# Performance work log

Measured on AMD Instinct MI355X. Metric: run time of the kernel, lower is better.

## Reference

```python
import jax, jax.numpy as jnp
import numpy as np

T, B, I, H, O = 256, 128, 512, 1024, 1


def setup_inputs() -> dict:
    key = jax.random.key(0)
    ks = jax.random.split(key, 7)
    s_ih = 1.0 / np.sqrt(H)
    return {
        "x": jax.random.normal(ks[0], (T, B, I), dtype=jnp.float32),
        "W_ih": jax.random.normal(ks[1], (H, I), dtype=jnp.float32) * s_ih,
        "W_hh": jax.random.normal(ks[2], (H, H), dtype=jnp.float32) * s_ih,
        "b_ih": jax.random.normal(ks[3], (H,), dtype=jnp.float32) * s_ih,
        "b_hh": jax.random.normal(ks[4], (H,), dtype=jnp.float32) * s_ih,
        "W_fc": jax.random.normal(ks[5], (O, H), dtype=jnp.float32) * s_ih,
        "b_fc": jax.random.normal(ks[6], (O,), dtype=jnp.float32) * s_ih,
    }


def reference(x, W_ih, W_hh, b_ih, b_hh, W_fc, b_fc):
    # Precompute the input projection for all timesteps at once: [T, B, H]
    xp = jnp.einsum("tbi,hi->tbh", x, W_ih) + b_ih + b_hh
    W_hh_T = W_hh.T  # [H, H]

    def step(h, xp_t):
        # h: [B, H]; torch nn.RNN uses tanh nonlinearity by default
        h_new = jnp.tanh(xp_t + h @ W_hh_T)
        return h_new, h_new

    h0 = jnp.zeros((B, H), dtype=x.dtype)  # hidden0 = zeros in the module
    _, hs = jax.lax.scan(step, h0, xp)  # hs: [T, B, H]

    # Linear head over every timestep's hidden state: [T, B, O]
    return jnp.einsum("tbh,oh->tbo", hs, W_fc) + b_fc
```

## Files before the change

kernel.cpp:

```cpp
#include <hip/hip_runtime.h>
#include <stdint.h>

typedef __attribute__((ext_vector_type(8))) short short8;
typedef __attribute__((ext_vector_type(4))) float f32x4;
typedef __attribute__((ext_vector_type(4))) unsigned int u32x4;
typedef __attribute__((ext_vector_type(2))) unsigned int u32x2;

__device__ __forceinline__ unsigned short f2bf(float f) {
  unsigned u = __float_as_uint(f);
  u += 0x7FFFu + ((u >> 16) & 1u);
  return (unsigned short)(u >> 16);
}
__device__ __forceinline__ float bf2f(unsigned short s) {
  return __uint_as_float(((unsigned)s) << 16);
}
__device__ __forceinline__ float ftanh(float x) {
  float e = __expf(2.0f * x);
  return 1.0f - 2.0f / (e + 1.0f);
}

__global__ __launch_bounds__(256) void cvt_kernel(const float* __restrict__ in,
                                                  unsigned short* __restrict__ out,
                                                  int n8) {
  int i = blockIdx.x * 256 + threadIdx.x;
  if (i >= n8) return;
  const float4* p = (const float4*)in + (size_t)i * 2;
  float4 a = p[0], b = p[1];
  uint4 o;
  o.x = (unsigned)f2bf(a.x) | ((unsigned)f2bf(a.y) << 16);
  o.y = (unsigned)f2bf(a.z) | ((unsigned)f2bf(a.w) << 16);
  o.z = (unsigned)f2bf(b.x) | ((unsigned)f2bf(b.y) << 16);
  o.w = (unsigned)f2bf(b.z) | ((unsigned)f2bf(b.w) << 16);
  ((uint4*)out)[i] = o;
}

__global__ __launch_bounds__(256) void scrub_kernel(unsigned* __restrict__ dst,
                                                    int n4) {
  int i = blockIdx.x * 256 + threadIdx.x;
  if (i >= n4) return;
  ((u32x4*)dst)[i] = (u32x4){0xAAAAAAAAu, 0xAAAAAAAAu, 0xAAAAAAAAu, 0xAAAAAAAAu};
}

__global__ __launch_bounds__(256) void gemm_xp(const unsigned short* __restrict__ A,
                                               const unsigned short* __restrict__ Bw,
                                               const float* __restrict__ b_ih,
                                               const float* __restrict__ b_hh,
                                               unsigned short* __restrict__ xp) {
  __shared__ unsigned short Al[8192];
  __shared__ unsigned short Bl[8192];
  int tid = threadIdx.x, lane = tid & 63, w = tid >> 6;
  int wm = w & 1, wn = w >> 1;
  int bx = blockIdx.x;
  int m0 = (bx >> 3) * 128, n0 = (bx & 7) * 128;

  f32x4 acc[4][4];
#pragma unroll
  for (int i = 0; i < 4; ++i)
#pragma unroll
    for (int jq = 0; jq < 4; ++jq) acc[i][jq] = (f32x4){0.f, 0.f, 0.f, 0.f};

  for (int kb = 0; kb < 512; kb += 64) {
#pragma unroll
    for (int i = 0; i < 4; ++i) {
      int S = (w * 4 + i) * 64 + lane;
      int row = S >> 3, pg = S & 7;
      int gk = ((pg ^ (row & 7)) << 3);
      const unsigned short* ga = A + (size_t)(m0 + row) * 512 + kb + gk;
      const unsigned short* gb = Bw + (size_t)(n0 + row) * 512 + kb + gk;
      __builtin_amdgcn_global_load_lds(
          (const __attribute__((address_space(1))) unsigned int*)ga,
          (__attribute__((address_space(3))) unsigned int*)&Al[(size_t)((w * 4 + i) * 64) * 8],
          16, 0, 0);
      __builtin_amdgcn_global_load_lds(
          (const __attribute__((address_space(1))) unsigned int*)gb,
          (__attribute__((address_space(3))) unsigned int*)&Bl[(size_t)((w * 4 + i) * 64) * 8],
          16, 0, 0);
    }
    asm volatile("s_waitcnt vmcnt(0)" ::: "memory");
    __syncthreads();

#pragma unroll
    for (int c = 0; c < 2; ++c) {
      short8 av[4], bv[4];
      int gg = c * 4 + (lane >> 4);
#pragma unroll
      for (int mt = 0; mt < 4; ++mt) {
        int rowa = wm * 64 + mt * 16 + (lane & 15);
        av[mt] = *(const short8*)&Al[(rowa * 8 + (gg ^ (rowa & 7))) * 8];
        int rowb = wn * 64 + mt * 16 + (lane & 15);
        bv[mt] = *(const short8*)&Bl[(rowb * 8 + (gg ^ (rowb & 7))) * 8];
      }
#pragma unroll
      for (int mt = 0; mt < 4; ++mt)
#pragma unroll
        for (int nt = 0; nt < 4; ++nt)
          acc[mt][nt] = __builtin_amdgcn_mfma_f32_16x16x32_bf16(av[mt], bv[nt], acc[mt][nt], 0, 0, 0);
    }
    __syncthreads();
  }

  int cl = lane & 15, qd = lane >> 4;
#pragma unroll
  for (int nt = 0; nt < 4; ++nt) {
    int col = n0 + wn * 64 + nt * 16 + cl;
    float bias = b_ih[col] + b_hh[col];
#pragma unroll
    for (int mt = 0; mt < 4; ++mt) {
#pragma unroll
      for (int r = 0; r < 4; ++r) {
        int m = m0 + wm * 64 + mt * 16 + qd * 4 + r;
        xp[(size_t)m * 1024 + col] = f2bf(acc[mt][nt][r] + bias);
      }
    }
  }
}

__global__ __launch_bounds__(512, 1) void scan_kernel(
    const float* __restrict__ Whh, const unsigned short* __restrict__ xp,
    const float* __restrict__ Wfc, const float* __restrict__ bfc,
    unsigned short* __restrict__ hs, float* __restrict__ out) {
  __shared__ __align__(16) unsigned short Abuf[2][2048 * 8];
  const int tid = threadIdx.x;
  const int lane = tid & 63, w = tid >> 6;
  const int g = blockIdx.x >> 3, p = blockIdx.x & 7;
  const int r = lane & 15, q = lane >> 4;
  const int b0 = g * 16;
  const int tile = p * 128 + w * 16;
  const int gcol = tile + r;
  const float bfcv = bfc[0];
  const float4 wfc4 = *(const float4*)(Wfc + tile + q * 4);
  const unsigned short* xlane = xp + (size_t)(b0 + r) * 1024 + tile + q * 4;

  int o0, o1, o2, o3;
  {
    int m, l, c, bb, q2;
    m = tid;         l = m & 63; c = m >> 6; bb = l & 15; q2 = l >> 4;
    o0 = (b0 + bb) * 1024 + c * 32 + q2 * 8;
    m = tid + 512;   l = m & 63; c = m >> 6; bb = l & 15; q2 = l >> 4;
    o1 = (b0 + bb) * 1024 + c * 32 + q2 * 8;
    m = tid + 1024;  l = m & 63; c = m >> 6; bb = l & 15; q2 = l >> 4;
    o2 = (b0 + bb) * 1024 + c * 32 + q2 * 8;
    m = tid + 1536;  l = m & 63; c = m >> 6; bb = l & 15; q2 = l >> 4;
    o3 = (b0 + bb) * 1024 + c * 32 + q2 * 8;
  }

  short8 Wf[32];
  {
    const float* wsrc = Whh + (size_t)gcol * 1024 + q * 8;
#pragma unroll
    for (int c = 0; c < 32; ++c) {
      float4 v0 = *(const float4*)(wsrc + c * 32);
      float4 v1 = *(const float4*)(wsrc + c * 32 + 4);
      short8 sv;
      sv[0] = (short)f2bf(v0.x); sv[1] = (short)f2bf(v0.y);
      sv[2] = (short)f2bf(v0.z); sv[3] = (short)f2bf(v0.w);
      sv[4] = (short)f2bf(v1.x); sv[5] = (short)f2bf(v1.y);
      sv[6] = (short)f2bf(v1.z); sv[7] = (short)f2bf(v1.w);
      Wf[c] = sv;
    }
  }

  {
#pragma unroll
    for (int i = 0; i < 4; ++i) {
      int m = tid + i * 512;
      int l = m & 63, c = m >> 6;
      int bb = l & 15, q2 = l >> 4;
      const unsigned short* src = xp + (size_t)(b0 + bb) * 1024 + c * 32 + q2 * 8;
      u32x4 xv = *(const u32x4*)src;
      const unsigned short* xs = (const unsigned short*)&xv;
      short8 sv;
      float pp = 0.f;
#pragma unroll
      for (int jj = 0; jj < 8; ++jj) {
        float h = ftanh(bf2f(xs[jj]));
        sv[jj] = (short)f2bf(h);
        pp += h * Wfc[c * 32 + q2 * 8 + jj];
      }
      *(short8*)&Abuf[1][(size_t)m * 8] = sv;
      if (p == 0) {
        if (m < 16) pp += bfcv;
        atomicAdd(out + b0 + bb, pp);
      }
    }
  }
  uint2 xw_next = *(const uint2*)(xlane + (size_t)1 * 131072);
  __syncthreads();

  u32x4 pv0, pv1, pv2, pv3;

  for (int s = 1; s < 256; ++s) {
    uint2 xw = xw_next;
    {
      int sn = (s < 255) ? s + 1 : 255;
      xw_next = *(const uint2*)(xlane + (size_t)sn * 131072);
    }

    unsigned short* curA = Abuf[s & 1];
    if (s >= 2) {
      asm volatile("s_waitcnt vmcnt(0)" ::: "memory");
      __builtin_amdgcn_sched_barrier(0);
      u32x4 v0 = pv0, v1 = pv1, v2 = pv2, v3 = pv3;
      const unsigned short* hbase = hs + (size_t)(s - 1) * 131072;
      const unsigned P = 0xAAAAAAAAu;
      int need =
          (v0[0] == P) | (v0[1] == P) | (v0[2] == P) | (v0[3] == P) |
          (v1[0] == P) | (v1[1] == P) | (v1[2] == P) | (v1[3] == P) |
          (v2[0] == P) | (v2[1] == P) | (v2[2] == P) | (v2[3] == P) |
          (v3[0] == P) | (v3[1] == P) | (v3[2] == P) | (v3[3] == P);
      int guard = 0;
      while (need) {
        asm volatile(
            "global_load_dwordx4 %0, %4, off sc1\n\t"
            "global_load_dwordx4 %1, %5, off sc1\n\t"
            "global_load_dwordx4 %2, %6, off sc1\n\t"
            "global_load_dwordx4 %3, %7, off sc1\n\t"
            "s_waitcnt vmcnt(0)"
            : "=&v"(v0), "=&v"(v1), "=&v"(v2), "=&v"(v3)
            : "v"((unsigned long long)(uintptr_t)(hbase + o0)),
              "v"((unsigned long long)(uintptr_t)(hbase + o1)),
              "v"((unsigned long long)(uintptr_t)(hbase + o2)),
              "v"((unsigned long long)(uintptr_t)(hbase + o3))
            : "memory");
        need =
            (v0[0] == P) | (v0[1] == P) | (v0[2] == P) | (v0[3] == P) |
            (v1[0] == P) | (v1[1] == P) | (v1[2] == P) | (v1[3] == P) |
            (v2[0] == P) | (v2[1] == P) | (v2[2] == P) | (v2[3] == P) |
            (v3[0] == P) | (v3[1] == P) | (v3[2] == P) | (v3[3] == P);
        if (++guard > (1 << 18)) break;
      }
      *(u32x4*)&curA[(size_t)(tid) * 8]          = v0;
      *(u32x4*)&curA[(size_t)(tid + 512) * 8]    = v1;
      *(u32x4*)&curA[(size_t)(tid + 1024) * 8]   = v2;
      *(u32x4*)&curA[(size_t)(tid + 1536) * 8]   = v3;
      __syncthreads();
    }

    f32x4 acc0 = (f32x4){0.f, 0.f, 0.f, 0.f};
    f32x4 acc1 = (f32x4){0.f, 0.f, 0.f, 0.f};
#pragma unroll
    for (int c = 0; c < 16; ++c) {
      short8 a0 = *(const short8*)&curA[(size_t)(2 * c) * 512 + lane * 8];
      short8 a1 = *(const short8*)&curA[(size_t)(2 * c + 1) * 512 + lane * 8];
      acc0 = __builtin_amdgcn_mfma_f32_16x16x32_bf16(Wf[2 * c], a0, acc0, 0, 0, 0);
      acc1 = __builtin_amdgcn_mfma_f32_16x16x32_bf16(Wf[2 * c + 1], a1, acc1, 0, 0, 0);
    }

    float h0 = ftanh(acc0[0] + acc1[0] + bf2f((unsigned short)(xw.x & 0xffff)));
    float h1 = ftanh(acc0[1] + acc1[1] + bf2f((unsigned short)(xw.x >> 16)));
    float h2 = ftanh(acc0[2] + acc1[2] + bf2f((unsigned short)(xw.y & 0xffff)));
    float h3 = ftanh(acc0[3] + acc1[3] + bf2f((unsigned short)(xw.y >> 16)));
    u32x2 dv;
    dv[0] = (unsigned)f2bf(h0) | ((unsigned)f2bf(h1) << 16);
    dv[1] = (unsigned)f2bf(h2) | ((unsigned)f2bf(h3) << 16);
    unsigned long long pa = (unsigned long long)(uintptr_t)(
        hs + ((size_t)s * 128 + b0 + r) * 1024 + tile + q * 4);
    asm volatile("global_store_dwordx2 %0, %1, off sc1"
                 :: "v"(pa), "v"(dv) : "memory");

    if (s < 255) {
      const unsigned short* hb = hs + (size_t)s * 131072;
      asm volatile(
          "global_load_dwordx4 %0, %4, off\n\t"
          "global_load_dwordx4 %1, %5, off\n\t"
          "global_load_dwordx4 %2, %6, off\n\t"
          "global_load_dwordx4 %3, %7, off"
          : "=&v"(pv0), "=&v"(pv1), "=&v"(pv2), "=&v"(pv3)
          : "v"((unsigned long long)(uintptr_t)(hb + o0)),
            "v"((unsigned long long)(uintptr_t)(hb + o1)),
            "v"((unsigned long long)(uintptr_t)(hb + o2)),
            "v"((unsigned long long)(uintptr_t)(hb + o3))
          : "memory");
    }

    float pp = h0 * wfc4.x + h1 * wfc4.y + h2 * wfc4.z + h3 * wfc4.w;
    pp += __shfl_xor(pp, 16, 64);
    pp += __shfl_xor(pp, 32, 64);
    if (lane < 16) {
      if (p == 0 && w == 0) pp += bfcv;
      atomicAdd(out + (size_t)s * 128 + b0 + lane, pp);
    }
  }
}

extern "C" void kernel_launch(void* const* d_in, const int* in_sizes, int n_in,
                              void* d_out, int out_size, void* d_ws, size_t ws_size,
                              hipStream_t stream) {
  (void)in_sizes; (void)n_in;
  const float* x   = (const float*)d_in[0];
  const float* Wih = (const float*)d_in[1];
  const float* Whh = (const float*)d_in[2];
  const float* bih = (const float*)d_in[3];
  const float* bhh = (const float*)d_in[4];
  const float* Wfc = (const float*)d_in[5];
  const float* bfc = (const float*)d_in[6];
  float* out = (float*)d_out;

  char* ws = (char*)d_ws;
  const bool big = ws_size >= (size_t)168820736;
  unsigned short* xp = (unsigned short*)(ws);
  unsigned short* hs = (unsigned short*)(ws + 67108864);
  unsigned short* xb = big ? (unsigned short*)(ws + 134217728)
                           : (unsigned short*)(ws + 67108864);
  unsigned short* wb = big ? (unsigned short*)(ws + 167772160)
                           : (unsigned short*)(ws + 100663296);

  hipMemsetAsync(out, 0, (size_t)out_size * 4, stream);

  cvt_kernel<<<8192, 256, 0, stream>>>(x, xb, 2097152);
  cvt_kernel<<<256, 256, 0, stream>>>(Wih, wb, 65536);
  gemm_xp<<<2048, 256, 0, stream>>>(xb, wb, bih, bhh, xp);
  if (!big) {
    scrub_kernel<<<8384, 256, 0, stream>>>(
        (unsigned*)(ws + 67108864 + 262144), 2146304);
  }
  scan_kernel<<<64, 512, 0, stream>>>(Whh, xp, Wfc, bfc, hs, out);
}
```

Before: 1.152 ms.

## Replace prefetch-then-spin with double-buffered pipelined polling of hidden-state flags

The early prefetch of the next step's hidden-state tile, issued right after the store, is removed. Each step now does a plain load of the tile. Only if a sentinel is still present does it enter a polling loop that keeps two sets of sc1 loads in flight, using vmcnt(4), so fresh samples arrive back to back and the loop exits wave-wide via __any. The __syncthreads is also replaced by an explicit lgkmcnt wait plus s_barrier. The aim is to cut the latency of detecting that the other blocks have published h, at the cost of more outstanding loads and a first plain load that may hit stale cached data.

```diff
diff --git a/kernel.cpp b/kernel.cpp
--- a/kernel.cpp
+++ b/kernel.cpp
@@ -114,6 +114,19 @@
     }
   }
 }
+
+#define CHKP(v) ((int)(((v)[0] == 0xAAAAAAAAu) | ((v)[1] == 0xAAAAAAAAu) | \
+                       ((v)[2] == 0xAAAAAAAAu) | ((v)[3] == 0xAAAAAAAAu)))
+
+#define SAMPLE_ISSUE(B0, B1, B2, B3)                                   \
+  asm volatile(                                                        \
+      "global_load_dwordx4 %0, %4, off sc1\n\t"                        \
+      "global_load_dwordx4 %1, %5, off sc1\n\t"                        \
+      "global_load_dwordx4 %2, %6, off sc1\n\t"                        \
+      "global_load_dwordx4 %3, %7, off sc1"                            \
+      : "+v"(B0), "+v"(B1), "+v"(B2), "+v"(B3)                         \
+      : "v"(a0), "v"(a1), "v"(a2), "v"(a3)                             \
+      : "memory")
 
 __global__ __launch_bounds__(512, 1) void scan_kernel(
     const float* __restrict__ Whh, const unsigned short* __restrict__ xp,
@@ -187,7 +200,8 @@
   uint2 xw_next = *(const uint2*)(xlane + (size_t)1 * 131072);
   __syncthreads();
 
-  u32x4 pv0, pv1, pv2, pv3;
+  u32x4 sa0 = {0,0,0,0}, sa1 = {0,0,0,0}, sa2 = {0,0,0,0}, sa3 = {0,0,0,0};
+  u32x4 sb0 = {0,0,0,0}, sb1 = {0,0,0,0}, sb2 = {0,0,0,0}, sb3 = {0,0,0,0};
 
   for (int s = 1; s < 256; ++s) {
     uint2 xw = xw_next;
@@ -198,52 +212,62 @@
 
     unsigned short* curA = Abuf[s & 1];
     if (s >= 2) {
-      asm volatile("s_waitcnt vmcnt(0)" ::: "memory");
-      __builtin_amdgcn_sched_barrier(0);
-      u32x4 v0 = pv0, v1 = pv1, v2 = pv2, v3 = pv3;
       const unsigned short* hbase = hs + (size_t)(s - 1) * 131072;
-      const unsigned P = 0xAAAAAAAAu;
-      int need =
-          (v0[0] == P) | (v0[1] == P) | (v0[2] == P) | (v0[3] == P) |
-          (v1[0] == P) | (v1[1] == P) | (v1[2] == P) | (v1[3] == P) |
-          (v2[0] == P) | (v2[1] == P) | (v2[2] == P) | (v2[3] == P) |
-          (v3[0] == P) | (v3[1] == P) | (v3[2] == P) | (v3[3] == P);
-      int guard = 0;
-      while (need) {
-        asm volatile(
-            "global_load_dwordx4 %0, %4, off sc1\n\t"
-            "global_load_dwordx4 %1, %5, off sc1\n\t"
-            "global_load_dwordx4 %2, %6, off sc1\n\t"
-            "global_load_dwordx4 %3, %7, off sc1\n\t"
-            "s_waitcnt vmcnt(0)"
-            : "=&v"(v0), "=&v"(v1), "=&v"(v2), "=&v"(v3)
-            : "v"((unsigned long long)(uintptr_t)(hbase + o0)),
-              "v"((unsigned long long)(uintptr_t)(hbase + o1)),
-              "v"((unsigned long long)(uintptr_t)(hbase + o2)),
-              "v"((unsigned long long)(uintptr_t)(hbase + o3))
-            : "memory");
-        need =
-            (v0[0] == P) | (v0[1] == P) | (v0[2] == P) | (v0[3] == P) |
-            (v1[0] == P) | (v1[1] == P) | (v1[2] == P) | (v1[3] == P) |
-            (v2[0] == P) | (v2[1] == P) | (v2[2] == P) | (v2[3] == P) |
-            (v3[0] == P) | (v3[1] == P) | (v3[2] == P) | (v3[3] == P);
-        if (++guard > (1 << 18)) break;
+      const u32x4* s0 = (const u32x4*)(hbase + o0);
+      const u32x4* s1 = (const u32x4*)(hbase + o1);
+      const u32x4* s2 = (const u32x4*)(hbase + o2);
+      const u32x4* s3 = (const u32x4*)(hbase + o3);
+      u32x4 v0 = *s0, v1 = *s1, v2 = *s2, v3 = *s3;
+      int need = CHKP(v0) | CHKP(v1) | CHKP(v2) | CHKP(v3);
+
+      if (__any(need)) {
+        const unsigned long long a0 = (unsigned long long)(uintptr_t)s0;
+        const unsigned long long a1 = (unsigned long long)(uintptr_t)s1;
+        const unsigned long long a2 = (unsigned long long)(uintptr_t)s2;
+        const unsigned long long a3 = (unsigned long long)(uintptr_t)s3;
+        SAMPLE_ISSUE(sa0, sa1, sa2, sa3);
+        SAMPLE_ISSUE(sb0, sb1, sb2, sb3);
+        int guard = 0;
+        for (;;) {
+          asm volatile("s_waitcnt vmcnt(4)" ::: "memory");
+          __builtin_amdgcn_sched_barrier(0);
+          if (need) {
+            if (!(CHKP(sa0) | CHKP(sa1) | CHKP(sa2) | CHKP(sa3))) {
+              v0 = sa0; v1 = sa1; v2 = sa2; v3 = sa3; need = 0;
+            }
+          }
+          if (!__any(need)) break;
+          SAMPLE_ISSUE(sa0, sa1, sa2, sa3);
+          asm volatile("s_waitcnt vmcnt(4)" ::: "memory");
+          __builtin_amdgcn_sched_barrier(0);
+          if (need) {
+            if (!(CHKP(sb0) | CHKP(sb1) | CHKP(sb2) | CHKP(sb3))) {
+              v0 = sb0; v1 = sb1; v2 = sb2; v3 = sb3; need = 0;
+            }
+          }
+          if (!__any(need)) break;
+          SAMPLE_ISSUE(sb0, sb1, sb2, sb3);
+          if (++guard > (1 << 17)) break;
+        }
       }
       *(u32x4*)&curA[(size_t)(tid) * 8]          = v0;
       *(u32x4*)&curA[(size_t)(tid + 512) * 8]    = v1;
       *(u32x4*)&curA[(size_t)(tid + 1024) * 8]   = v2;
       *(u32x4*)&curA[(size_t)(tid + 1536) * 8]   = v3;
-      __syncthreads();
+      asm volatile("s_waitcnt lgkmcnt(0)" ::: "memory");
+      __builtin_amdgcn_sched_barrier(0);
+      __builtin_amdgcn_s_barrier();
+      __builtin_amdgcn_sched_barrier(0);
     }
 
     f32x4 acc0 = (f32x4){0.f, 0.f, 0.f, 0.f};
     f32x4 acc1 = (f32x4){0.f, 0.f, 0.f, 0.f};
 #pragma unroll
     for (int c = 0; c < 16; ++c) {
-      short8 a0 = *(const short8*)&curA[(size_t)(2 * c) * 512 + lane * 8];
-      short8 a1 = *(const short8*)&curA[(size_t)(2 * c + 1) * 512 + lane * 8];
-      acc0 = __builtin_amdgcn_mfma_f32_16x16x32_bf16(Wf[2 * c], a0, acc0, 0, 0, 0);
-      acc1 = __builtin_amdgcn_mfma_f32_16x16x32_bf16(Wf[2 * c + 1], a1, acc1, 0, 0, 0);
+      short8 a0v = *(const short8*)&curA[(size_t)(2 * c) * 512 + lane * 8];
+      short8 a1v = *(const short8*)&curA[(size_t)(2 * c + 1) * 512 + lane * 8];
+      acc0 = __builtin_amdgcn_mfma_f32_16x16x32_bf16(Wf[2 * c], a0v, acc0, 0, 0, 0);
+      acc1 = __builtin_amdgcn_mfma_f32_16x16x32_bf16(Wf[2 * c + 1], a1v, acc1, 0, 0, 0);
     }
 
     float h0 = ftanh(acc0[0] + acc1[0] + bf2f((unsigned short)(xw.x & 0xffff)));
@@ -257,21 +281,6 @@
         hs + ((size_t)s * 128 + b0 + r) * 1024 + tile + q * 4);
     asm volatile("global_store_dwordx2 %0, %1, off sc1"
                  :: "v"(pa), "v"(dv) : "memory");
-
-    if (s < 255) {
-      const unsigned short* hb = hs + (size_t)s * 131072;
-      asm volatile(
-          "global_load_dwordx4 %0, %4, off\n\t"
-          "global_load_dwordx4 %1, %5, off\n\t"
-          "global_load_dwordx4 %2, %6, off\n\t"
-          "global_load_dwordx4 %3, %7, off"
-          : "=&v"(pv0), "=&v"(pv1), "=&v"(pv2), "=&v"(pv3)
-          : "v"((unsigned long long)(uintptr_t)(hb + o0)),
-            "v"((unsigned long long)(uintptr_t)(hb + o1)),
-            "v"((unsigned long long)(uintptr_t)(hb + o2)),
-            "v"((unsigned long long)(uintptr_t)(hb + o3))
-          : "memory");
-    }
 
     float pp = h0 * wfc4.x + h1 * wfc4.y + h2 * wfc4.z + h3 * wfc4.w;
     pp += __shfl_xor(pp, 16, 64);
```

Result: faster. 1.117 ms (-3.0%).
